# Performance work log

Hardware: AMD Instinct MI355X
Metric: run time of the kernel (lower is better)

## Reference

```python
import jax, jax.numpy as jnp
import numpy as np

LOG_2PI = float(np.log(2.0 * np.pi))


def setup_inputs() -> dict:
    key = jax.random.key(0)
    k1, k2, k3 = jax.random.split(key, 3)
    N, D, K = 2_000_000, 16, 32
    data = jax.random.normal(k1, (N, D), dtype=jnp.float32)
    means = jax.random.uniform(k2, (K, D), dtype=jnp.float32)  # torch.rand init
    # torch init is eye expanded per component; perturb slightly so the
    # Cholesky / solve paths are exercised with non-trivial values while
    # A @ A.T stays well-conditioned PD.
    cov_parts = (jnp.eye(D, dtype=jnp.float32)[None, :, :]
                 + 0.1 * jax.random.normal(k3, (K, D, D), dtype=jnp.float32))
    log_weights = jnp.zeros((K,), dtype=jnp.float32)
    return {"data": data, "means": means, "cov_parts": cov_parts,
            "log_weights": log_weights}


def _mixture_loglik(data, means, cov_parts, log_weights):
    D = data.shape[-1]
    # covariance_k = A_k @ A_k^T  -> Cholesky factor L_k (lower)
    cov = jnp.einsum('kij,klj->kil', cov_parts, cov_parts)      # [K, D, D]
    chol = jnp.linalg.cholesky(cov)                             # [K, D, D]

    def comp_logprob(mu, L):
        # MVN log_prob for one component over all N points
        diff = data - mu                                        # [N, D]
        # solve L z = diff^T  -> z: [D, N]
        z = jax.scipy.linalg.solve_triangular(L, diff.T, lower=True)
        quad = jnp.sum(z * z, axis=0)                           # [N]
        logdet = jnp.sum(jnp.log(jnp.diagonal(L)))              # 0.5*logdet(cov)
        return -0.5 * (quad + D * LOG_2PI) - logdet             # [N]

    # [N, K] log-likelihood per point per component
    log_liks = jax.vmap(comp_logprob, in_axes=(0, 0), out_axes=1)(means, chol)
    weighted = log_liks + log_weights ** 2                      # note: squared, per source
    return jnp.mean(jax.nn.logsumexp(weighted, axis=1))


def reference(data, means, cov_parts, log_weights):
    return _mixture_loglik(data, means, cov_parts, log_weights)
```

## Files before the change

kernel.cpp:

```cpp
#include <hip/hip_runtime.h>
#include <math.h>


#define LOG_2PI 1.8378770664093453f
#define INV_LN2 1.4426950408889634f
#define LN2_D   0.6931471805599453

typedef float    float4v __attribute__((ext_vector_type(4)));
typedef float    f32x16  __attribute__((ext_vector_type(16)));
typedef _Float16 f16x8   __attribute__((ext_vector_type(8)));
typedef _Float16 f16x2   __attribute__((ext_vector_type(2)));

union H8 { f16x8 h8; f16x2 h2[4]; };

#if __has_builtin(__builtin_amdgcn_exp2f)
#define EXP2F(x) __builtin_amdgcn_exp2f(x)
#else
#define EXP2F(x) exp2f(x)
#endif
#if __has_builtin(__builtin_amdgcn_logf)
#define LOG2F(x) __builtin_amdgcn_logf(x)
#else
#define LOG2F(x) log2f(x)
#endif

static __device__ __forceinline__ f16x2 pk2(float a, float b) {
#if __has_builtin(__builtin_amdgcn_cvt_pkrtz)
  return __builtin_bit_cast(f16x2, __builtin_amdgcn_cvt_pkrtz(a, b));
#else
  f16x2 r; r[0] = (_Float16)a; r[1] = (_Float16)b; return r;
#endif
}

static __device__ __forceinline__ float partner32(float x, bool lo) {
#if __has_builtin(__builtin_amdgcn_permlane32_swap)
  typedef unsigned u32x2 __attribute__((ext_vector_type(2)));
  unsigned u = __builtin_bit_cast(unsigned, x);
  u32x2 r = __builtin_amdgcn_permlane32_swap(u, u, false, false);
  return __builtin_bit_cast(float, lo ? r[1] : r[0]);
#else
  return __shfl_xor(x, 32, 64);
#endif
}

__global__ void setup_kernel(const float* __restrict__ means,
                             const float* __restrict__ cov_parts,
                             const float* __restrict__ log_weights,
                             _Float16* __restrict__ W,
                             float* __restrict__ c2)
{
  const int k = blockIdx.x;
  const int i = threadIdx.x;

  __shared__ float sA[16][17];
  __shared__ float sC[16][17];
  __shared__ float sMu[16];
  __shared__ float sR[16];

  if (i < 16) {
    #pragma unroll
    for (int j = 0; j < 16; ++j) sA[i][j] = cov_parts[(k*16 + i)*16 + j];
    sMu[i] = means[k*16 + i];
  }
  __syncthreads();

  if (i < 16) {
    #pragma unroll
    for (int j = 0; j < 16; ++j) {
      float acc = 0.f;
      #pragma unroll
      for (int l = 0; l < 16; ++l) acc += sA[i][l] * sA[j][l];
      sC[i][j] = acc;
    }
  }
  __syncthreads();

  for (int j = 0; j < 16; ++j) {
    if (i == j) {
      float d = sC[j][j];
      for (int l = 0; l < j; ++l) d -= sC[j][l]*sC[j][l];
      sC[j][j] = sqrtf(d);
    }
    __syncthreads();
    if (i < 16 && i > j) {
      float a = sC[i][j];
      for (int l = 0; l < j; ++l) a -= sC[i][l]*sC[j][l];
      sC[i][j] = a / sC[j][j];
    }
    __syncthreads();
  }

  if (i < 16) {
    float y[16];
    #pragma unroll
    for (int r = 0; r < 16; ++r) {
      float a = (r == i) ? 1.f : 0.f;
      #pragma unroll
      for (int l = 0; l < r; ++l) a -= sC[r][l] * y[l];
      y[r] = a / sC[r][r];
    }
    #pragma unroll
    for (int r = 0; r < 16; ++r) sA[r][i] = y[r];
  }
  __syncthreads();

  if (i < 16) {
    float p[16];
    #pragma unroll
    for (int j = 0; j < 16; ++j) {
      float acc = 0.f;
      #pragma unroll
      for (int l = 0; l < 16; ++l) acc += sA[l][i] * sA[l][j];
      p[j] = acc;
    }
    float ri = 0.f;
    #pragma unroll
    for (int j = 0; j < 16; ++j) ri += p[j] * sMu[j];
    sR[i] = ri;

    #pragma unroll
    for (int j = 0; j < 16; ++j) {
      W[(size_t)(i*64 + (k + 32*(j >> 3)))*8 + (j & 7)] =
          (_Float16)(-0.5f * INV_LN2 * p[j]);
    }
    W[(size_t)(16*64 + (k + 32*(i >> 3)))*8 + (i & 7)] =
        (_Float16)(INV_LN2 * ri);
  }
  __syncthreads();

  if (i == 0) {
    float logdet = 0.f;
    #pragma unroll
    for (int j = 0; j < 16; ++j) logdet += __logf(sC[j][j]);
    float mupmu = 0.f;
    #pragma unroll
    for (int j = 0; j < 16; ++j) mupmu += sMu[j] * sR[j];
    float lw = log_weights[k];
    c2[k] = INV_LN2 * (-0.5f*(mupmu + 16.f*LOG_2PI) - logdet + lw*lw);
  }
}

__global__ __launch_bounds__(256, 3) void main_kernel(
    const float* __restrict__ data,
    const _Float16* __restrict__ W,
    const float* __restrict__ c2,
    float* __restrict__ partials,
    int npts, int ntiles)
{
  const int lane = threadIdx.x & 63;
  const int n32  = lane & 31;
  const bool lo  = lane < 32;
  const int h    = lo ? 0 : 1;
  const int gwave  = (int)((blockIdx.x * blockDim.x + threadIdx.x) >> 6);
  const int nwaves = (int)((gridDim.x * blockDim.x) >> 6);

  f16x8 Wf[17];
  #pragma unroll
  for (int c = 0; c < 17; ++c)
    Wf[c] = *(const f16x8*)(W + (size_t)(c*64 + lane)*8);

  float c2r[16];
  #pragma unroll
  for (int r = 0; r < 16; ++r)
    c2r[r] = c2[(r & 3) + 8*(r >> 2) + 4*h];

  float accsum = 0.f;

  float4v p0, p1, p2, p3;
  if (gwave < ntiles) {
    const float* xp = data + ((size_t)gwave*32 + n32)*16;
    p0 = *(const float4v*)(xp);
    p1 = *(const float4v*)(xp + 4);
    p2 = *(const float4v*)(xp + 8);
    p3 = *(const float4v*)(xp + 12);
  }

  for (int tile = gwave; tile < ntiles; tile += nwaves) {
    float x[16];
    #pragma unroll
    for (int j = 0; j < 4; ++j) {
      x[j] = p0[j]; x[4+j] = p1[j]; x[8+j] = p2[j]; x[12+j] = p3[j];
    }
    int nt = tile + nwaves;
    if (nt < ntiles) {
      const float* xp = data + ((size_t)nt*32 + n32)*16;
      p0 = *(const float4v*)(xp);
      p1 = *(const float4v*)(xp + 4);
      p2 = *(const float4v*)(xp + 8);
      p3 = *(const float4v*)(xp + 12);
    }

    f16x2 xselh[4];
    #pragma unroll
    for (int j = 0; j < 4; ++j) {
      unsigned ulo = __builtin_bit_cast(unsigned, pk2(x[2*j],   x[2*j+1]));
      unsigned uhi = __builtin_bit_cast(unsigned, pk2(x[8+2*j], x[9+2*j]));
      xselh[j] = __builtin_bit_cast(f16x2, lo ? ulo : uhi);
    }

    f32x16 acc;
    #pragma unroll
    for (int r = 0; r < 16; ++r) acc[r] = 0.f;

    #pragma unroll
    for (int c = 0; c < 16; ++c) {
      f16x2 xi2 = pk2(x[c], x[c]);
      H8 b;
      #pragma unroll
      for (int j = 0; j < 4; ++j) b.h2[j] = xi2 * xselh[j];
      acc = __builtin_amdgcn_mfma_f32_32x32x16_f16(Wf[c], b.h8, acc, 0, 0, 0);
    }
    {
      H8 b;
      #pragma unroll
      for (int j = 0; j < 4; ++j) b.h2[j] = xselh[j];
      acc = __builtin_amdgcn_mfma_f32_32x32x16_f16(Wf[16], b.h8, acc, 0, 0, 0);
    }

    float v[16];
    #pragma unroll
    for (int r = 0; r < 16; ++r) v[r] = acc[r] + c2r[r];
    float m = v[0];
    #pragma unroll
    for (int r = 1; r < 16; ++r) m = fmaxf(m, v[r]);
    m = fmaxf(m, partner32(m, lo));
    float s = 0.f;
    #pragma unroll
    for (int r = 0; r < 16; ++r) s += EXP2F(v[r] - m);
    s += partner32(s, lo);
    accsum += m + LOG2F(s);
  }

  #pragma unroll
  for (int off = 1; off <= 32; off <<= 1)
    accsum += __shfl_xor(accsum, off, 64);

  __shared__ float wsum[4];
  const int wid = (int)(threadIdx.x >> 6);
  if ((threadIdx.x & 63) == 0) wsum[wid] = accsum;
  __syncthreads();
  if (threadIdx.x == 0)
    partials[blockIdx.x] = wsum[0] + wsum[1] + wsum[2] + wsum[3];
}

__global__ void reduce_kernel(const float* __restrict__ partials, int n,
                              float* __restrict__ out, double scale)
{
  __shared__ double sd[256];
  double a = 0.0;
  for (int idx = threadIdx.x; idx < n; idx += 256) a += (double)partials[idx];
  sd[threadIdx.x] = a;
  __syncthreads();
  for (int s = 128; s > 0; s >>= 1) {
    if ((int)threadIdx.x < s) sd[threadIdx.x] += sd[threadIdx.x + s];
    __syncthreads();
  }
  if (threadIdx.x == 0) out[0] = (float)(sd[0] * scale);
}

extern "C" void kernel_launch(void* const* d_in, const int* in_sizes, int n_in,
                              void* d_out, int out_size, void* d_ws, size_t ws_size,
                              hipStream_t stream)
{
  const float* data        = (const float*)d_in[0];
  const float* means       = (const float*)d_in[1];
  const float* cov_parts   = (const float*)d_in[2];
  const float* log_weights = (const float*)d_in[3];

  const int npts   = in_sizes[0] / 16;
  const int ntiles = npts / 32;

  _Float16* W      = (_Float16*)d_ws;
  float*    c2     = (float*)((char*)d_ws + (size_t)17*64*8*sizeof(_Float16));
  float*    partials = c2 + 32;

  const int GRID = 1536, BLOCK = 256;
  setup_kernel<<<32, 64, 0, stream>>>(means, cov_parts, log_weights, W, c2);
  main_kernel<<<GRID, BLOCK, 0, stream>>>(data, W, c2, partials, npts, ntiles);
  reduce_kernel<<<1, 256, 0, stream>>>(partials, GRID, (float*)d_out,
                                       LN2_D / (2.0 * (double)npts));
}
```

Baseline: 204.4 us.

## Stage MFMA weights in LDS and process two tiles per wave iteration

```diff
diff --git a/kernel.cpp b/kernel.cpp
--- a/kernel.cpp
+++ b/kernel.cpp
@@ -147,6 +147,17 @@
     float* __restrict__ partials,
     int npts, int ntiles)
 {
+  __shared__ _Float16 sW[17*64*8];
+  __shared__ float wsum[4];
+
+  {
+    const float4v* src = (const float4v*)W;
+    float4v* dst = (float4v*)sW;
+    for (int idx = threadIdx.x; idx < 17*64*8/8; idx += 256)
+      dst[idx] = src[idx];
+  }
+  __syncthreads();
+
   const int lane = threadIdx.x & 63;
   const int n32  = lane & 31;
   const bool lo  = lane < 32;
@@ -154,88 +165,119 @@
   const int gwave  = (int)((blockIdx.x * blockDim.x + threadIdx.x) >> 6);
   const int nwaves = (int)((gridDim.x * blockDim.x) >> 6);
 
-  f16x8 Wf[17];
-  #pragma unroll
-  for (int c = 0; c < 17; ++c)
-    Wf[c] = *(const f16x8*)(W + (size_t)(c*64 + lane)*8);
+  const _Float16* sWl = sW + (size_t)lane*8;
 
   float c2r[16];
   #pragma unroll
   for (int r = 0; r < 16; ++r)
     c2r[r] = c2[(r & 3) + 8*(r >> 2) + 4*h];
 
+  const int npairs = (ntiles + 1) >> 1;
   float accsum = 0.f;
 
-  float4v p0, p1, p2, p3;
-  if (gwave < ntiles) {
-    const float* xp = data + ((size_t)gwave*32 + n32)*16;
-    p0 = *(const float4v*)(xp);
-    p1 = *(const float4v*)(xp + 4);
-    p2 = *(const float4v*)(xp + 8);
-    p3 = *(const float4v*)(xp + 12);
-  }
-
-  for (int tile = gwave; tile < ntiles; tile += nwaves) {
-    float x[16];
+  float4v pA0, pA1, pA2, pA3, pB0, pB1, pB2, pB3;
+  if (gwave < npairs) {
+    int tA = 2*gwave, tB = (2*gwave+1 < ntiles) ? 2*gwave+1 : 2*gwave;
+    const float* xa = data + ((size_t)tA*32 + n32)*16;
+    const float* xb = data + ((size_t)tB*32 + n32)*16;
+    pA0 = *(const float4v*)(xa);    pA1 = *(const float4v*)(xa + 4);
+    pA2 = *(const float4v*)(xa + 8); pA3 = *(const float4v*)(xa + 12);
+    pB0 = *(const float4v*)(xb);    pB1 = *(const float4v*)(xb + 4);
+    pB2 = *(const float4v*)(xb + 8); pB3 = *(const float4v*)(xb + 12);
+  }
+
+  for (int p = gwave; p < npairs; p += nwaves) {
+    float xA[16], xB[16];
     #pragma unroll
     for (int j = 0; j < 4; ++j) {
-      x[j] = p0[j]; x[4+j] = p1[j]; x[8+j] = p2[j]; x[12+j] = p3[j];
-    }
-    int nt = tile + nwaves;
-    if (nt < ntiles) {
-      const float* xp = data + ((size_t)nt*32 + n32)*16;
-      p0 = *(const float4v*)(xp);
-      p1 = *(const float4v*)(xp + 4);
-      p2 = *(const float4v*)(xp + 8);
-      p3 = *(const float4v*)(xp + 12);
-    }
-
-    f16x2 xselh[4];
+      xA[j] = pA0[j]; xA[4+j] = pA1[j]; xA[8+j] = pA2[j]; xA[12+j] = pA3[j];
+      xB[j] = pB0[j]; xB[4+j] = pB1[j]; xB[8+j] = pB2[j]; xB[12+j] = pB3[j];
+    }
+    const bool validB = (2*p+1 < ntiles);
+
+    int np_ = p + nwaves;
+    if (np_ < npairs) {
+      int tA = 2*np_, tB = (2*np_+1 < ntiles) ? 2*np_+1 : 2*np_;
+      const float* xa = data + ((size_t)tA*32 + n32)*16;
+      const float* xb = data + ((size_t)tB*32 + n32)*16;
+      pA0 = *(const float4v*)(xa);    pA1 = *(const float4v*)(xa + 4);
+      pA2 = *(const float4v*)(xa + 8); pA3 = *(const float4v*)(xa + 12);
+      pB0 = *(const float4v*)(xb);    pB1 = *(const float4v*)(xb + 4);
+      pB2 = *(const float4v*)(xb + 8); pB3 = *(const float4v*)(xb + 12);
+    }
+
+    f16x2 xsA[4], xsB[4];
     #pragma unroll
     for (int j = 0; j < 4; ++j) {
-      unsigned ulo = __builtin_bit_cast(unsigned, pk2(x[2*j],   x[2*j+1]));
-      unsigned uhi = __builtin_bit_cast(unsigned, pk2(x[8+2*j], x[9+2*j]));
-      xselh[j] = __builtin_bit_cast(f16x2, lo ? ulo : uhi);
-    }
-
-    f32x16 acc;
-    #pragma unroll
-    for (int r = 0; r < 16; ++r) acc[r] = 0.f;
+      unsigned la = __builtin_bit_cast(unsigned, pk2(xA[2*j],   xA[2*j+1]));
+      unsigned ha = __builtin_bit_cast(unsigned, pk2(xA[8+2*j], xA[9+2*j]));
+      xsA[j] = __builtin_bit_cast(f16x2, lo ? la : ha);
+      unsigned lb = __builtin_bit_cast(unsigned, pk2(xB[2*j],   xB[2*j+1]));
+      unsigned hb = __builtin_bit_cast(unsigned, pk2(xB[8+2*j], xB[9+2*j]));
+      xsB[j] = __builtin_bit_cast(f16x2, lo ? lb : hb);
+    }
+
+    f32x16 accA, accB;
+    #pragma unroll
+    for (int r = 0; r < 16; ++r) { accA[r] = 0.f; accB[r] = 0.f; }
 
     #pragma unroll
     for (int c = 0; c < 16; ++c) {
-      f16x2 xi2 = pk2(x[c], x[c]);
-      H8 b;
-      #pragma unroll
-      for (int j = 0; j < 4; ++j) b.h2[j] = xi2 * xselh[j];
-      acc = __builtin_amdgcn_mfma_f32_32x32x16_f16(Wf[c], b.h8, acc, 0, 0, 0);
+      f16x8 wc = *(const f16x8*)(sWl + (size_t)c*512);
+      f16x2 xa2 = pk2(xA[c], xA[c]);
+      H8 bA;
+      #pragma unroll
+      for (int j = 0; j < 4; ++j) bA.h2[j] = xa2 * xsA[j];
+      accA = __builtin_amdgcn_mfma_f32_32x32x16_f16(wc, bA.h8, accA, 0, 0, 0);
+      f16x2 xb2 = pk2(xB[c], xB[c]);
+      H8 bB;
+      #pragma unroll
+      for (int j = 0; j < 4; ++j) bB.h2[j] = xb2 * xsB[j];
+      accB = __builtin_amdgcn_mfma_f32_32x32x16_f16(wc, bB.h8, accB, 0, 0, 0);
     }
     {
-      H8 b;
-      #pragma unroll
-      for (int j = 0; j < 4; ++j) b.h2[j] = xselh[j];
-      acc = __builtin_amdgcn_mfma_f32_32x32x16_f16(Wf[16], b.h8, acc, 0, 0, 0);
-    }
-
-    float v[16];
-    #pragma unroll
-    for (int r = 0; r < 16; ++r) v[r] = acc[r] + c2r[r];
-    float m = v[0];
-    #pragma unroll
-    for (int r = 1; r < 16; ++r) m = fmaxf(m, v[r]);
-    m = fmaxf(m, partner32(m, lo));
-    float s = 0.f;
-    #pragma unroll
-    for (int r = 0; r < 16; ++r) s += EXP2F(v[r] - m);
-    s += partner32(s, lo);
-    accsum += m + LOG2F(s);
+      f16x8 wc = *(const f16x8*)(sWl + (size_t)16*512);
+      H8 bA, bB;
+      #pragma unroll
+      for (int j = 0; j < 4; ++j) { bA.h2[j] = xsA[j]; bB.h2[j] = xsB[j]; }
+      accA = __builtin_amdgcn_mfma_f32_32x32x16_f16(wc, bA.h8, accA, 0, 0, 0);
+      accB = __builtin_amdgcn_mfma_f32_32x32x16_f16(wc, bB.h8, accB, 0, 0, 0);
+    }
+
+    {
+      float v[16];
+      #pragma unroll
+      for (int r = 0; r < 16; ++r) v[r] = accA[r] + c2r[r];
+      float m = v[0];
+      #pragma unroll
+      for (int r = 1; r < 16; ++r) m = fmaxf(m, v[r]);
+      m = fmaxf(m, partner32(m, lo));
+      float s = 0.f;
+      #pragma unroll
+      for (int r = 0; r < 16; ++r) s += EXP2F(v[r] - m);
+      s += partner32(s, lo);
+      accsum += m + LOG2F(s);
+    }
+    {
+      float v[16];
+      #pragma unroll
+      for (int r = 0; r < 16; ++r) v[r] = accB[r] + c2r[r];
+      float m = v[0];
+      #pragma unroll
+      for (int r = 1; r < 16; ++r) m = fmaxf(m, v[r]);
+      m = fmaxf(m, partner32(m, lo));
+      float s = 0.f;
+      #pragma unroll
+      for (int r = 0; r < 16; ++r) s += EXP2F(v[r] - m);
+      s += partner32(s, lo);
+      accsum += validB ? (m + LOG2F(s)) : 0.f;
+    }
   }
 
   #pragma unroll
   for (int off = 1; off <= 32; off <<= 1)
     accsum += __shfl_xor(accsum, off, 64);
 
-  __shared__ float wsum[4];
   const int wid = (int)(threadIdx.x >> 6);
   if ((threadIdx.x & 63) == 0) wsum[wid] = accsum;
   __syncthreads();
@@ -268,13 +310,13 @@
   const float* log_weights = (const float*)d_in[3];
 
   const int npts   = in_sizes[0] / 16;
-  const int ntiles = npts / 32;
+  const int ntiles = (npts + 31) / 32;
 
   _Float16* W      = (_Float16*)d_ws;
   float*    c2     = (float*)((char*)d_ws + (size_t)17*64*8*sizeof(_Float16));
   float*    partials = c2 + 32;
 
-  const int GRID = 1536, BLOCK = 256;
+  const int GRID = 768, BLOCK = 256;
   setup_kernel<<<32, 64, 0, stream>>>(means, cov_parts, log_weights, W, c2);
   main_kernel<<<GRID, BLOCK, 0, stream>>>(data, W, c2, partials, npts, ntiles);
   reduce_kernel<<<1, 256, 0, stream>>>(partials, GRID, (float*)d_out,
```

After: 260.4 us. 1.27x slower.
